# Optimization experiments

Measured on AMD Instinct MI355X. Metric: run time of the kernel, lower is better.

The kernel has to match this reference:

```python
import jax, jax.numpy as jnp
import numpy as np

NBINS = 10
POOL = 8
MAX_ANGLE = float(np.pi)


def _sobel_weight(dtype):
    m = jnp.array([[1.0, 0.0, -1.0], [2.0, 0.0, -2.0], [1.0, 0.0, -1.0]], dtype=dtype)
    # [2, 1, 3, 3]: channel 0 = m, channel 1 = m.T
    return jnp.stack([m, m.T], axis=0)[:, None, :, :]


def setup_inputs() -> dict:
    key = jax.random.key(0)
    x = jax.random.uniform(key, (16, 1, 512, 512), dtype=jnp.float32)
    return {"x": x}


def reference(x):
    w = _sobel_weight(x.dtype)
    # conv2d, stride 1, padding 1 -> gxy: [N, 2, H, W]
    gxy = jax.lax.conv_general_dilated(
        x, w, window_strides=(1, 1), padding=[(1, 1), (1, 1)],
        dimension_numbers=("NCHW", "OIHW", "NCHW"))
    gx = gxy[:, 0]  # [N, H, W]
    gy = gxy[:, 1]
    mag = jnp.sqrt(gx * gx + gy * gy)          # gxy.norm(dim=1)
    phase = jnp.arctan2(gx, gy)
    phase_int = phase / MAX_ANGLE * NBINS      # [N, H, W]
    fl = jnp.mod(jnp.floor(phase_int).astype(jnp.int32), NBINS)
    ce = jnp.mod(jnp.ceil(phase_int).astype(jnp.int32), NBINS)
    # scatter_(set) on zeros then scatter_add_ == sum of two one-hot weighted terms
    oh_f = jax.nn.one_hot(fl, NBINS, dtype=x.dtype, axis=1)  # [N, NBINS, H, W]
    oh_c = jax.nn.one_hot(ce, NBINS, dtype=x.dtype, axis=1)
    out = oh_f * mag[:, None] + oh_c * (1.0 - mag)[:, None]  # [N, NBINS, H, W]
    # AvgPool2d(POOL, stride=POOL)
    n, c, h, wdt = out.shape
    pooled = out.reshape(n, c, h // POOL, POOL, wdt // POOL, POOL).mean(axis=(3, 5))
    return pooled
```

## Files before the change

### kernel.cpp

```cpp
#include <hip/hip_runtime.h>
#include <math.h>

#define THR_BASE 9.42477e-5f
#define KFOLD 256.0f
#define KFOLD_INV 0.00390625f

#define LOADROW_P(DST, RR)                                                \
    {                                                                     \
        int rr = (RR);                                                    \
        bool rok = (rr >= 0) && (rr < 512);                               \
        const float* rp = img + (size_t)(rok ? rr : row0) * 512;          \
        const float4* rp4 = (const float4*)(rp + col0);                   \
        float4 v0 = rp4[0], v1 = rp4[1];                                  \
        float lf = rp[(cw > 0) ? (col0 - 1) : col0];                      \
        float rt = rp[(cw < 63) ? (col0 + 8) : col0];                     \
        float m = rok ? 1.0f : 0.0f;                                      \
        DST[0] = (cw > 0 && rok) ? lf : 0.0f;                             \
        DST[1] = v0.x * m; DST[2] = v0.y * m;                             \
        DST[3] = v0.z * m; DST[4] = v0.w * m;                             \
        DST[5] = v1.x * m; DST[6] = v1.y * m;                             \
        DST[7] = v1.z * m; DST[8] = v1.w * m;                             \
        DST[9] = (cw < 63 && rok) ? rt : 0.0f;                            \
    }

#define LOADROW_F(DST, RR)                                                \
    {                                                                     \
        const float* rp = img + (size_t)(RR) * 512;                       \
        const float4* rp4 = (const float4*)(rp + col0);                   \
        float4 v0 = rp4[0], v1 = rp4[1];                                  \
        DST[0] = rp[col0 - 1];                                            \
        DST[1] = v0.x; DST[2] = v0.y; DST[3] = v0.z; DST[4] = v0.w;       \
        DST[5] = v1.x; DST[6] = v1.y; DST[7] = v1.z; DST[8] = v1.w;       \
        DST[9] = rp[col0 + 8];                                            \
    }

__global__ void __launch_bounds__(256) hog_kernel(const float* __restrict__ x,
                                                  float* __restrict__ out) {
    int t    = blockIdx.x * 256 + threadIdx.x;
    int r2   = t & 3;
    int cell = t >> 2;
    int cw   = cell & 63;
    int ch   = (cell >> 6) & 63;
    int n    = cell >> 12;

    const float* img = x + (size_t)n * (512 * 512);
    int row0 = ch * 8 + r2 * 2;
    int col0 = cw * 8;

    float dd0[10], dd1[10], uu0[10], uu1[10];
    {
        float t0[10], t1[10], t2[10], t3[10];
        bool border = (cw == 0) | (cw == 63)
                    | ((ch == 0) & (r2 == 0)) | ((ch == 63) & (r2 == 3));
        if (__any((int)border)) {
            LOADROW_P(t0, row0 - 1)
            LOADROW_P(t1, row0)
            LOADROW_P(t2, row0 + 1)
            LOADROW_P(t3, row0 + 2)
        } else {
            LOADROW_F(t0, row0 - 1)
            LOADROW_F(t1, row0)
            LOADROW_F(t2, row0 + 1)
            LOADROW_F(t3, row0 + 2)
        }
#pragma unroll
        for (int c = 0; c < 10; ++c) {
            dd0[c] = fmaf(2.0f, t1[c], t0[c] + t2[c]);
            dd1[c] = fmaf(2.0f, t2[c], t1[c] + t3[c]);
            uu0[c] = t0[c] - t2[c];
            uu1[c] = t1[c] - t3[c];
        }
    }

    float gx[16], gy[16];
#pragma unroll
    for (int c = 0; c < 8; ++c) {
        gx[c]     = dd0[c] - dd0[c + 2];
        gx[8 + c] = dd1[c] - dd1[c + 2];
        gy[c]     = fmaf(2.0f, uu0[c + 1], uu0[c] + uu0[c + 2]);
        gy[8 + c] = fmaf(2.0f, uu1[c + 1], uu1[c] + uu1[c + 2]);
    }

    float accA[5], accB[5];
#pragma unroll
    for (int j = 0; j < 5; ++j) { accA[j] = 0.0f; accB[j] = 0.0f; }
    unsigned bmask = 0u;

#pragma unroll
    for (int p = 0; p < 16; ++p) {
        float gxc = gx[p], gyc = gy[p];
        float mag = __builtin_amdgcn_sqrtf(fmaf(gxc, gxc, gyc * gyc));
        float a = fabsf(gxc), b = fabsf(gyc);

        float m1 = fmaf(a, 0.95105651629515353f, -(b * 0.30901699437494740f));
        float m2 = fmaf(a, 0.80901699437494745f, -(b * 0.58778525229247314f));
        float m3 = fmaf(a, 0.58778525229247314f, -(b * 0.80901699437494745f));
        float m4 = fmaf(a, 0.30901699437494740f, -(b * 0.95105651629515353f));

        int k1 = __float_as_int(m1) >> 31;
        int k2 = __float_as_int(m2) >> 31;
        int k3 = __float_as_int(m3) >> 31;
        int k4 = __float_as_int(m4) >> 31;
        int qm = (__float_as_int(gxc) ^ __float_as_int(gyc)) >> 31;

        float magK = mag + KFOLD;
        float magA = __int_as_float(__float_as_int(magK) & ~qm);
        float magB = magK - magA;

        accA[0] += magA;
        accB[0] += magB;
        accA[1] += __int_as_float(__float_as_int(magA) & ~k1);
        accB[1] += __int_as_float(__float_as_int(magB) & ~k1);
        accA[2] += __int_as_float(__float_as_int(magA) & ~k2);
        accB[2] += __int_as_float(__float_as_int(magB) & ~k2);
        accA[3] += __int_as_float(__float_as_int(magA) & ~k3);
        accB[3] += __int_as_float(__float_as_int(magB) & ~k3);
        accA[4] += __int_as_float(__float_as_int(magA) & ~k4);
        accB[4] += __int_as_float(__float_as_int(magB) & ~k4);

        float dmin = fminf(fminf(fminf(fabsf(m1), fabsf(m2)),
                                 fminf(fabsf(m3), fabsf(m4))),
                           fminf(a, b));
        bmask = (dmin < THR_BASE * fmaxf(mag, 1.0f)) ? (bmask | (1u << p)) : bmask;
    }

    while (__any((int)(bmask != 0u))) {
        if (bmask) {
            int p = (int)__builtin_ctz(bmask);
            bmask &= bmask - 1u;
            int prow = row0 + (p >> 3);
            int pc   = col0 + (p & 7);
            int rm = prow - 1, rq = prow + 1;
            int cm = pc - 1, cp = pc + 1;
            bool rmok = rm >= 0, rqok = rq < 512;
            bool cmok = cm >= 0, cpok = cp < 512;
            float w00 = (rmok && cmok) ? img[(size_t)rm * 512 + cm] : 0.0f;
            float w01 = rmok ? img[(size_t)rm * 512 + pc] : 0.0f;
            float w02 = (rmok && cpok) ? img[(size_t)rm * 512 + cp] : 0.0f;
            float w10 = cmok ? img[(size_t)prow * 512 + cm] : 0.0f;
            float w12 = cpok ? img[(size_t)prow * 512 + cp] : 0.0f;
            float w20 = (rqok && cmok) ? img[(size_t)rq * 512 + cm] : 0.0f;
            float w21 = rqok ? img[(size_t)rq * 512 + pc] : 0.0f;
            float w22 = (rqok && cpok) ? img[(size_t)rq * 512 + cp] : 0.0f;

            float gxf = fmaf(2.0f, w10, w00 + w20) - fmaf(2.0f, w12, w02 + w22);
            float gyf = fmaf(2.0f, w01 - w21, (w00 - w20) + (w02 - w22));
            float magf = __builtin_amdgcn_sqrtf(fmaf(gxf, gxf, gyf * gyf));
            int negf = (int)(__float_as_uint(fmaf(fabsf(gxf), 0.95105651629515353f, -(fabsf(gyf) * 0.30901699437494740f))) >> 31)
                     + (int)(__float_as_uint(fmaf(fabsf(gxf), 0.80901699437494745f, -(fabsf(gyf) * 0.58778525229247314f))) >> 31)
                     + (int)(__float_as_uint(fmaf(fabsf(gxf), 0.58778525229247314f, -(fabsf(gyf) * 0.80901699437494745f))) >> 31)
                     + (int)(__float_as_uint(fmaf(fabsf(gxf), 0.30901699437494740f, -(fabsf(gyf) * 0.95105651629515353f))) >> 31);
            bool qqf = (((__float_as_uint(gxf) ^ __float_as_uint(gyf)) >> 31) != 0u);
            int onesf = 4 - negf;

            float uv = -(magf + KFOLD);
#pragma unroll
            for (int j = 0; j < 5; ++j) {
                accA[j] += (!qqf && j <= onesf) ? uv : 0.0f;
                accB[j] += ( qqf && j <= onesf) ? uv : 0.0f;
            }

            double gxd = (((((double)w00 - (double)w02) + 2.0 * (double)w10)
                           - 2.0 * (double)w12) + (double)w20) - (double)w22;
            double gyd = (((((double)w00 + 2.0 * (double)w01) + (double)w02)
                           - (double)w20) - 2.0 * (double)w21) - (double)w22;
            bool sideB;
            int onese;
            float mvals;
            if (gxd == 0.0) {
                sideB = false; onese = 0; mvals = 1.0f;
            } else if (gyd == 0.0) {
                sideB = true; onese = 4; mvals = 1.0f;
            } else {
                double ad = fabs(gxd), bd = fabs(gyd);
                double M1 = fma(ad, 0.95105651629515353118, -(bd * 0.30901699437494742410));
                double M2 = fma(ad, 0.80901699437494742410, -(bd * 0.58778525229247312917));
                double M3 = fma(ad, 0.58778525229247312917, -(bd * 0.80901699437494742410));
                double M4 = fma(ad, 0.30901699437494742410, -(bd * 0.95105651629515353118));
                int negd = (int)(M1 < 0.0) + (int)(M2 < 0.0)
                         + (int)(M3 < 0.0) + (int)(M4 < 0.0);
                sideB = (gxd < 0.0) != (gyd < 0.0);
                onese = 4 - negd;
                mvals = magf;
            }
            float av = mvals + KFOLD;
#pragma unroll
            for (int j = 0; j < 5; ++j) {
                accA[j] += (!sideB && j <= onese) ? av : 0.0f;
                accB[j] += ( sideB && j <= onese) ? av : 0.0f;
            }
        }
    }

    float Am[5], An[5], Bm[5], Bn[5];
#pragma unroll
    for (int j = 0; j < 5; ++j) {
        float qa = rintf(accA[j] * KFOLD_INV);
        Am[j] = fmaf(qa, -KFOLD, accA[j]);
        An[j] = qa;
        float qb = rintf(accB[j] * KFOLD_INV);
        Bm[j] = fmaf(qb, -KFOLD, accB[j]);
        Bn[j] = qb;
    }
    float M[10], C[10];
#pragma unroll
    for (int s = 0; s < 5; ++s) {
        float am1 = (s < 4) ? Am[s + 1] : 0.0f;
        float an1 = (s < 4) ? An[s + 1] : 0.0f;
        M[s] = Am[s] - am1;
        C[s] = An[s] - an1;
        float bm1 = (s < 4) ? Bm[s + 1] : 0.0f;
        float bn1 = (s < 4) ? Bn[s + 1] : 0.0f;
        M[9 - s] = Bm[s] - bm1;
        C[9 - s] = Bn[s] - bn1;
    }

    float* op = out + (((size_t)n * 10) * 64 + ch) * 64 + cw;
#pragma unroll
    for (int b = 0; b < 10; ++b) {
        int bm1 = (b + 9) % 10;
        float v = (M[b] - M[bm1]) + C[bm1];
        v += __shfl_xor(v, 1);
        v += __shfl_xor(v, 2);
        if (r2 == 0) op[(size_t)b * 4096] = v * (1.0f / 64.0f);
    }
}

extern "C" void kernel_launch(void* const* d_in, const int* in_sizes, int n_in,
                              void* d_out, int out_size, void* d_ws, size_t ws_size,
                              hipStream_t stream) {
    const float* x = (const float*)d_in[0];
    float* out = (float*)d_out;
    const int total = 16 * 64 * 64 * 4;
    hog_kernel<<<total / 256, 256, 0, stream>>>(x, out);
}
```

Measured before the change: 17.60 us.

## Stage a 10-row image band in LDS per block instead of per-thread global loads

```diff
diff --git a/kernel.cpp b/kernel.cpp
--- a/kernel.cpp
+++ b/kernel.cpp
@@ -4,72 +4,72 @@
 #define THR_BASE 9.42477e-5f
 #define KFOLD 256.0f
 #define KFOLD_INV 0.00390625f
-
-#define LOADROW_P(DST, RR)                                                \
-    {                                                                     \
-        int rr = (RR);                                                    \
-        bool rok = (rr >= 0) && (rr < 512);                               \
-        const float* rp = img + (size_t)(rok ? rr : row0) * 512;          \
-        const float4* rp4 = (const float4*)(rp + col0);                   \
-        float4 v0 = rp4[0], v1 = rp4[1];                                  \
-        float lf = rp[(cw > 0) ? (col0 - 1) : col0];                      \
-        float rt = rp[(cw < 63) ? (col0 + 8) : col0];                     \
-        float m = rok ? 1.0f : 0.0f;                                      \
-        DST[0] = (cw > 0 && rok) ? lf : 0.0f;                             \
-        DST[1] = v0.x * m; DST[2] = v0.y * m;                             \
-        DST[3] = v0.z * m; DST[4] = v0.w * m;                             \
-        DST[5] = v1.x * m; DST[6] = v1.y * m;                             \
-        DST[7] = v1.z * m; DST[8] = v1.w * m;                             \
-        DST[9] = (cw < 63 && rok) ? rt : 0.0f;                            \
-    }
-
-#define LOADROW_F(DST, RR)                                                \
-    {                                                                     \
-        const float* rp = img + (size_t)(RR) * 512;                       \
-        const float4* rp4 = (const float4*)(rp + col0);                   \
-        float4 v0 = rp4[0], v1 = rp4[1];                                  \
-        DST[0] = rp[col0 - 1];                                            \
-        DST[1] = v0.x; DST[2] = v0.y; DST[3] = v0.z; DST[4] = v0.w;       \
-        DST[5] = v1.x; DST[6] = v1.y; DST[7] = v1.z; DST[8] = v1.w;       \
-        DST[9] = rp[col0 + 8];                                            \
-    }
+#define LSTRIDE 532
 
 __global__ void __launch_bounds__(256) hog_kernel(const float* __restrict__ x,
                                                   float* __restrict__ out) {
-    int t    = blockIdx.x * 256 + threadIdx.x;
-    int r2   = t & 3;
-    int cell = t >> 2;
-    int cw   = cell & 63;
-    int ch   = (cell >> 6) & 63;
-    int n    = cell >> 12;
-
+    __shared__ float s[10 * LSTRIDE];
+
+    int tid = threadIdx.x;
+    int blk = blockIdx.x;
+    int ch  = blk & 63;
+    int n   = blk >> 6;
     const float* img = x + (size_t)n * (512 * 512);
+    int R0 = ch * 8 - 1;
+
+#pragma unroll
+    for (int k = 0; k < 5; ++k) {
+        int j = tid + k * 256;
+        int lrow = j >> 7;
+        int cb = j & 127;
+        int R = R0 + lrow;
+        bool rok = (R >= 0) && (R < 512);
+        const float4* gp = (const float4*)(img + (size_t)(rok ? R : 0) * 512) + cb;
+        float4 v = *gp;
+        float m = rok ? 1.0f : 0.0f;
+        int L = lrow * LSTRIDE + 5 + cb * 4;
+        s[L + 0] = v.x * m;
+        s[L + 1] = v.y * m;
+        s[L + 2] = v.z * m;
+        s[L + 3] = v.w * m;
+    }
+    if (tid < 10) {
+        s[tid * LSTRIDE + 4]   = 0.0f;
+        s[tid * LSTRIDE + 517] = 0.0f;
+    }
+    __syncthreads();
+
+    int r2   = tid & 3;
+    int cw   = tid >> 2;
     int row0 = ch * 8 + r2 * 2;
     int col0 = cw * 8;
 
+    float t0[10], t1[10], t2[10], t3[10];
+    {
+        int base = (2 * r2) * LSTRIDE + 8 * cw + 4;
+#define READROW(DST, D)                                                   \
+        {                                                                 \
+            const float* rp = &s[base + (D) * LSTRIDE];                   \
+            float4 a4 = *(const float4*)(rp);                             \
+            float4 b4 = *(const float4*)(rp + 4);                         \
+            DST[0] = a4.x; DST[1] = a4.y; DST[2] = a4.z; DST[3] = a4.w;   \
+            DST[4] = b4.x; DST[5] = b4.y; DST[6] = b4.z; DST[7] = b4.w;   \
+            DST[8] = rp[8]; DST[9] = rp[9];                               \
+        }
+        READROW(t0, 0)
+        READROW(t1, 1)
+        READROW(t2, 2)
+        READROW(t3, 3)
+#undef READROW
+    }
+
     float dd0[10], dd1[10], uu0[10], uu1[10];
-    {
-        float t0[10], t1[10], t2[10], t3[10];
-        bool border = (cw == 0) | (cw == 63)
-                    | ((ch == 0) & (r2 == 0)) | ((ch == 63) & (r2 == 3));
-        if (__any((int)border)) {
-            LOADROW_P(t0, row0 - 1)
-            LOADROW_P(t1, row0)
-            LOADROW_P(t2, row0 + 1)
-            LOADROW_P(t3, row0 + 2)
-        } else {
-            LOADROW_F(t0, row0 - 1)
-            LOADROW_F(t1, row0)
-            LOADROW_F(t2, row0 + 1)
-            LOADROW_F(t3, row0 + 2)
-        }
-#pragma unroll
-        for (int c = 0; c < 10; ++c) {
-            dd0[c] = fmaf(2.0f, t1[c], t0[c] + t2[c]);
-            dd1[c] = fmaf(2.0f, t2[c], t1[c] + t3[c]);
-            uu0[c] = t0[c] - t2[c];
-            uu1[c] = t1[c] - t3[c];
-        }
+#pragma unroll
+    for (int c = 0; c < 10; ++c) {
+        dd0[c] = fmaf(2.0f, t1[c], t0[c] + t2[c]);
+        dd1[c] = fmaf(2.0f, t2[c], t1[c] + t3[c]);
+        uu0[c] = t0[c] - t2[c];
+        uu1[c] = t1[c] - t3[c];
     }
 
     float gx[16], gy[16];
@@ -118,9 +118,8 @@
         accA[4] += __int_as_float(__float_as_int(magA) & ~k4);
         accB[4] += __int_as_float(__float_as_int(magB) & ~k4);
 
-        float dmin = fminf(fminf(fminf(fabsf(m1), fabsf(m2)),
-                                 fminf(fabsf(m3), fabsf(m4))),
-                           fminf(a, b));
+        float dmin = fminf(fminf(fminf(fabsf(m1), fabsf(m2)), fabsf(m3)),
+                           fminf(fminf(fabsf(m4), a), b));
         bmask = (dmin < THR_BASE * fmaxf(mag, 1.0f)) ? (bmask | (1u << p)) : bmask;
     }
 
@@ -204,15 +203,15 @@
     }
     float M[10], C[10];
 #pragma unroll
-    for (int s = 0; s < 5; ++s) {
-        float am1 = (s < 4) ? Am[s + 1] : 0.0f;
-        float an1 = (s < 4) ? An[s + 1] : 0.0f;
-        M[s] = Am[s] - am1;
-        C[s] = An[s] - an1;
-        float bm1 = (s < 4) ? Bm[s + 1] : 0.0f;
-        float bn1 = (s < 4) ? Bn[s + 1] : 0.0f;
-        M[9 - s] = Bm[s] - bm1;
-        C[9 - s] = Bn[s] - bn1;
+    for (int sdx = 0; sdx < 5; ++sdx) {
+        float am1 = (sdx < 4) ? Am[sdx + 1] : 0.0f;
+        float an1 = (sdx < 4) ? An[sdx + 1] : 0.0f;
+        M[sdx] = Am[sdx] - am1;
+        C[sdx] = An[sdx] - an1;
+        float bm1 = (sdx < 4) ? Bm[sdx + 1] : 0.0f;
+        float bn1 = (sdx < 4) ? Bn[sdx + 1] : 0.0f;
+        M[9 - sdx] = Bm[sdx] - bm1;
+        C[9 - sdx] = Bn[sdx] - bn1;
     }
 
     float* op = out + (((size_t)n * 10) * 64 + ch) * 64 + cw;
```

Measured after the change: 16.57 us. 1.06x faster.
